# Optimization experiments

Hardware: AMD Instinct MI355X
Metric: run time of the kernel (lower is better)

The kernel has to match this reference:

```python
import jax, jax.numpy as jnp
import numpy as np

N = 50000
E = 600000
D = 128


def gcn_conv(x, row, col, w, W, b):
    """PyG GCNConv: add self-loops (weight 1), symmetric deg^-1/2 normalization,
    linear transform, edge-weighted scatter-add aggregation, then bias."""
    n = x.shape[0]
    loop = jnp.arange(n)
    r = jnp.concatenate([row, loop])            # source nodes, [E+N]
    c = jnp.concatenate([col, loop])            # target nodes, [E+N]
    ww = jnp.concatenate([w, jnp.ones((n,), x.dtype)])
    deg = jax.ops.segment_sum(ww, c, num_segments=n)          # weighted in-degree
    dinv = jnp.where(deg > 0, jax.lax.rsqrt(deg), jnp.zeros_like(deg))
    norm = dinv[r] * ww * dinv[c]               # [E+N]
    xl = x @ W                                  # [n, D_out]
    msg = norm[:, None] * xl[r]                 # gather + scale, [E+N, D_out]
    out = jax.ops.segment_sum(msg, c, num_segments=n)
    return out + b


def setup_inputs() -> dict:
    key = jax.random.key(0)
    ks = jax.random.split(key, 12)
    x = jax.random.normal(ks[0], (N, D), dtype=jnp.float32)
    edge_index = jax.random.randint(ks[1], (2, E), 0, N, dtype=jnp.int64)
    edge_weights = jax.random.uniform(ks[2], (E,), dtype=jnp.float32)
    s = 1.0 / np.sqrt(D)
    W1 = jax.random.uniform(ks[3], (D, D), jnp.float32, -s, s)
    b1 = jnp.zeros((D,), jnp.float32)
    W2 = jax.random.uniform(ks[4], (D, D), jnp.float32, -s, s)
    b2 = jnp.zeros((D,), jnp.float32)
    W3 = jax.random.uniform(ks[5], (D, D), jnp.float32, -s, s)
    b3 = jnp.zeros((D,), jnp.float32)
    prelu_w = jnp.array(0.25, jnp.float32)
    return {"x": x, "edge_index": edge_index, "edge_weights": edge_weights,
            "W1": W1, "b1": b1, "W2": W2, "b2": b2, "W3": W3, "b3": b3,
            "prelu_w": prelu_w}


def reference(x, edge_index, edge_weights, W1, b1, W2, b2, W3, b3, prelu_w):
    row, col = edge_index[0], edge_index[1]
    # layer 1: GCNConv -> (dropout: eval, identity) -> ELU
    h = gcn_conv(x, row, col, edge_weights, W1, b1)
    h = jax.nn.elu(h)
    # layer 2: GCNConv -> GELU (torch default = exact erf)
    h = gcn_conv(h, row, col, edge_weights, W2, b2)
    h = jax.nn.gelu(h, approximate=False)
    # layer 3: GCNConv -> PReLU (learnable scalar slope)
    h = gcn_conv(h, row, col, edge_weights, W3, b3)
    h = jnp.where(h >= 0, h, prelu_w * h)
    return h
```

## Files before the change

kernel.cpp:

```cpp
#include <hip/hip_runtime.h>
#include <hip/hip_fp16.h>
#include <math.h>

constexpr int D = 128;

struct __align__(16) H8 { __half2 h[4]; };
struct __align__(8)  H4 { __half2 a, b; };

typedef _Float16 half8 __attribute__((ext_vector_type(8)));
typedef float    floatx4 __attribute__((ext_vector_type(4)));


__device__ __forceinline__ int detect64(const int* __restrict__ ei) {
  int z = 0;
#pragma unroll
  for (int i = 0; i < 8; ++i) z |= ei[2 * i + 1];
  return (z == 0) ? 1 : 0;
}

__device__ __forceinline__ void load_edge(const int* __restrict__ ei, int e, int nE,
                                          int m64, int n, int& r, int& c) {
  if (m64) { r = ei[2 * (size_t)e]; c = ei[2 * ((size_t)nE + e)]; }
  else     { r = ei[(size_t)e];     c = ei[(size_t)nE + e]; }
  r = min(max(r, 0), n - 1);
  c = min(max(c, 0), n - 1);
}

__global__ void k_zero(int* __restrict__ cnt, int n) {
  int i = blockIdx.x * blockDim.x + threadIdx.x;
  if (i < n) cnt[i] = 0;
}

__global__ void k_pos(const int* __restrict__ ei, int* __restrict__ cnt,
                      int2* __restrict__ rc, int* __restrict__ pos, int nE, int n) {
  int e = blockIdx.x * blockDim.x + threadIdx.x;
  if (e >= nE) return;
  int m64 = detect64(ei);
  int r, c;
  load_edge(ei, e, nE, m64, n, r, c);
  rc[e] = make_int2(r, c);
  pos[e] = atomicAdd(&cnt[c], 1);
}

__global__ void k_scan1(const int* __restrict__ cnt, int* __restrict__ offs,
                        int* __restrict__ bsum, int n) {
  __shared__ int s[256];
  int t = threadIdx.x;
  int i = blockIdx.x * 256 + t;
  int v = (i < n) ? cnt[i] : 0;
  s[t] = v;
  __syncthreads();
  for (int off = 1; off < 256; off <<= 1) {
    int x = 0;
    if (t >= off) x = s[t - off];
    __syncthreads();
    if (t >= off) s[t] += x;
    __syncthreads();
  }
  if (i < n) offs[i] = s[t] - v;
  if (t == 255) bsum[blockIdx.x] = s[255];
}

__global__ void k_scan2(const int* __restrict__ bsum, int* __restrict__ boff, int nb) {
  __shared__ int s[256];
  int t = threadIdx.x;
  int v = (t < nb) ? bsum[t] : 0;
  s[t] = v;
  __syncthreads();
  for (int off = 1; off < 256; off <<= 1) {
    int x = 0;
    if (t >= off) x = s[t - off];
    __syncthreads();
    if (t >= off) s[t] += x;
    __syncthreads();
  }
  if (t < nb) boff[t] = s[t] - v;
}

__global__ void k_scan3(int* __restrict__ offs, const int* __restrict__ boff, int n, int nE) {
  int i = blockIdx.x * 256 + threadIdx.x;
  if (i < n) offs[i] += boff[blockIdx.x];
  if (i == 0) offs[n] = nE;
}

__global__ void k_fill(const int2* __restrict__ rc, const int* __restrict__ pos,
                       const float* __restrict__ w, const int* __restrict__ offs,
                       int2* __restrict__ ecf, int nE) {
  int e = blockIdx.x * blockDim.x + threadIdx.x;
  if (e >= nE) return;
  int2 p = rc[e];
  int idx = offs[p.y] + pos[e];
  ecf[idx] = make_int2(p.x, __float_as_int(w[e]));
}

__global__ void k_degdinv(const int2* __restrict__ ecf, const int* __restrict__ offs,
                          float* __restrict__ dinv, int n) {
  int i = blockIdx.x * blockDim.x + threadIdx.x;
  if (i >= n) return;
  float s = 1.0f;
  int e1 = offs[i + 1];
  for (int e = offs[i]; e < e1; ++e) s += __int_as_float(ecf[e].y);
  dinv[i] = rsqrtf(s);
}

__global__ void k_coef(const int2* __restrict__ ecf, const float* __restrict__ dinv,
                       unsigned int* __restrict__ ecf2, int nE) {
  int e = blockIdx.x * blockDim.x + threadIdx.x;
  if (e >= nE) return;
  int2 p = ecf[e];
  float c = dinv[p.x] * __int_as_float(p.y);
  ecf2[e] = ((unsigned int)p.x << 16) |
            (unsigned int)__half_as_ushort(__float2half_rn(c));
}

__global__ void k_wt(const float* __restrict__ W1, const float* __restrict__ W2,
                     const float* __restrict__ W3, __half* __restrict__ Wt) {
  __shared__ float s[128][129];
  const float* W = blockIdx.x == 0 ? W1 : (blockIdx.x == 1 ? W2 : W3);
  __half* o = Wt + (size_t)blockIdx.x * D * D;
  int tid = threadIdx.x;
#pragma unroll
  for (int i = 0; i < 16; ++i) {
    int flat = i * 1024 + tid * 4;
    int k = flat >> 7;
    int nn = flat & 127;
    float4 v = *(const float4*)(W + (size_t)k * D + nn);
    s[k][nn] = v.x; s[k][nn + 1] = v.y; s[k][nn + 2] = v.z; s[k][nn + 3] = v.w;
  }
  __syncthreads();
#pragma unroll
  for (int i = 0; i < 8; ++i) {
    int flat = i * 256 + tid;
    int nn = flat >> 4;
    int k0 = (flat & 15) * 8;
    H8 hv;
#pragma unroll
    for (int t = 0; t < 4; ++t)
      hv.h[t] = __floats2half2_rn(s[k0 + 2 * t][nn], s[k0 + 2 * t + 1][nn]);
    *(H8*)(o + (size_t)nn * D + k0) = hv;
  }
}

template <int ACT>
__device__ __forceinline__ float act_f(float x) {
  if (ACT == 1) return x > 0.f ? x : expm1f(x);
  if (ACT == 2) return 0.5f * x * (1.0f + erff(x * 0.70710678118654752440f));
  return x;
}

template <int ACT, typename AT>
__global__ __launch_bounds__(256) void k_gemm(const AT* __restrict__ A,
                                              const __half* __restrict__ Wt,
                                              __half* __restrict__ Y, int n) {
  const int wave = threadIdx.x >> 6;
  const int lane = threadIdx.x & 63;
  const int np = lane & 15;
  const int quad = lane >> 4;
  const int node = blockIdx.x * 64 + wave * 16 + np;
  const int nc = min(node, n - 1);

  half8 b[4];
#pragma unroll
  for (int s = 0; s < 4; ++s) {
    if constexpr (sizeof(AT) == 4) {
      const float* ap = (const float*)A + (size_t)nc * D + s * 32 + quad * 8;
      float4 v0 = *(const float4*)ap;
      float4 v1 = *(const float4*)(ap + 4);
      b[s][0] = (_Float16)act_f<ACT>(v0.x); b[s][1] = (_Float16)act_f<ACT>(v0.y);
      b[s][2] = (_Float16)act_f<ACT>(v0.z); b[s][3] = (_Float16)act_f<ACT>(v0.w);
      b[s][4] = (_Float16)act_f<ACT>(v1.x); b[s][5] = (_Float16)act_f<ACT>(v1.y);
      b[s][6] = (_Float16)act_f<ACT>(v1.z); b[s][7] = (_Float16)act_f<ACT>(v1.w);
    } else {
      half8 raw = *(const half8*)((const __half*)A + ((size_t)s * n + nc) * 32 + quad * 8);
#pragma unroll
      for (int t = 0; t < 8; ++t)
        b[s][t] = (_Float16)act_f<ACT>((float)raw[t]);
    }
  }

  floatx4 acc[8];
#pragma unroll
  for (int mt = 0; mt < 8; ++mt) acc[mt] = (floatx4){0.f, 0.f, 0.f, 0.f};

#pragma unroll
  for (int mt = 0; mt < 8; ++mt) {
#pragma unroll
    for (int s = 0; s < 4; ++s) {
      half8 a = *(const half8*)(Wt + (size_t)(mt * 16 + np) * D + s * 32 + quad * 8);
      acc[mt] = __builtin_amdgcn_mfma_f32_16x16x32_f16(a, b[s], acc[mt], 0, 0, 0);
    }
  }

  if (node < n) {
#pragma unroll
    for (int mt = 0; mt < 8; ++mt) {
      H4 hv;
      hv.a = __floats2half2_rn(acc[mt][0], acc[mt][1]);
      hv.b = __floats2half2_rn(acc[mt][2], acc[mt][3]);
      int f0 = mt * 16 + quad * 4;
      *(H4*)(Y + ((size_t)(f0 >> 5) * n + node) * 32 + (f0 & 31)) = hv;
    }
  }
}

__device__ __forceinline__ void fmacc8(float* acc, float c, const H8& y) {
  float2 f;
  f = __half22float2(y.h[0]); acc[0] += c * f.x; acc[1] += c * f.y;
  f = __half22float2(y.h[1]); acc[2] += c * f.x; acc[3] += c * f.y;
  f = __half22float2(y.h[2]); acc[4] += c * f.x; acc[5] += c * f.y;
  f = __half22float2(y.h[3]); acc[6] += c * f.x; acc[7] += c * f.y;
}

__device__ __forceinline__ float cdecode(unsigned int u) {
  return __half2float(__ushort_as_half((unsigned short)(u & 0xffffu)));
}

template <int PRELU, typename OutT>
__global__ __launch_bounds__(256) void k_agg(const __half* __restrict__ Y,
                                             const int* __restrict__ offs,
                                             const unsigned int* __restrict__ ecf2,
                                             const float* __restrict__ dinv,
                                             const float* __restrict__ bias,
                                             const float* __restrict__ pw,
                                             OutT* __restrict__ OUT, int n) {
  const int chunk = blockIdx.x & 3;
  const int t = threadIdx.x;
  const int node = (blockIdx.x >> 2) * 32 + (t >> 3);
  const int sub = (t >> 2) & 1;
  const int j = t & 3;
  if (node >= n) return;
  const __half* Yc = Y + (size_t)chunk * n * 32;
  float dc = dinv[node];
  float acc[8] = {0.f, 0.f, 0.f, 0.f, 0.f, 0.f, 0.f, 0.f};
  if (sub == 0) {
    H8 ys = *(const H8*)(Yc + (size_t)node * 32 + j * 8);
    fmacc8(acc, dc, ys);
  }
  int e0 = offs[node], e1 = offs[node + 1];
  int e = e0 + sub;
  for (; e + 6 < e1; e += 8) {
    unsigned int u0 = ecf2[e], u1 = ecf2[e + 2], u2 = ecf2[e + 4], u3 = ecf2[e + 6];
    H8 y0 = *(const H8*)(Yc + (size_t)(u0 >> 16) * 32 + j * 8);
    H8 y1 = *(const H8*)(Yc + (size_t)(u1 >> 16) * 32 + j * 8);
    H8 y2 = *(const H8*)(Yc + (size_t)(u2 >> 16) * 32 + j * 8);
    H8 y3 = *(const H8*)(Yc + (size_t)(u3 >> 16) * 32 + j * 8);
    fmacc8(acc, cdecode(u0), y0);
    fmacc8(acc, cdecode(u1), y1);
    fmacc8(acc, cdecode(u2), y2);
    fmacc8(acc, cdecode(u3), y3);
  }
  for (; e < e1; e += 2) {
    unsigned int u = ecf2[e];
    H8 y = *(const H8*)(Yc + (size_t)(u >> 16) * 32 + j * 8);
    fmacc8(acc, cdecode(u), y);
  }
#pragma unroll
  for (int i = 0; i < 8; ++i) acc[i] += __shfl_xor(acc[i], 4, 64);
  float4 b4 = *(const float4*)(bias + chunk * 32 + j * 8 + sub * 4);
  float o[4];
  o[0] = dc * acc[sub * 4 + 0] + b4.x;
  o[1] = dc * acc[sub * 4 + 1] + b4.y;
  o[2] = dc * acc[sub * 4 + 2] + b4.z;
  o[3] = dc * acc[sub * 4 + 3] + b4.w;
  if (PRELU) {
    float wv = *pw;
#pragma unroll
    for (int i = 0; i < 4; ++i) o[i] = o[i] >= 0.f ? o[i] : wv * o[i];
  }
  if constexpr (sizeof(OutT) == 4) {
    *(float4*)((float*)OUT + (size_t)node * D + chunk * 32 + j * 8 + sub * 4) =
        make_float4(o[0], o[1], o[2], o[3]);
  } else {
    H4 hv;
    hv.a = __floats2half2_rn(o[0], o[1]);
    hv.b = __floats2half2_rn(o[2], o[3]);
    *(H4*)((__half*)OUT + ((size_t)chunk * n + node) * 32 + j * 8 + sub * 4) = hv;
  }
}

extern "C" void kernel_launch(void* const* d_in, const int* in_sizes, int n_in,
                              void* d_out, int out_size, void* d_ws, size_t ws_size,
                              hipStream_t stream) {
  const float* x  = (const float*)d_in[0];
  const int*   ei = (const int*)d_in[1];
  const float* w  = (const float*)d_in[2];
  const float* W1 = (const float*)d_in[3];
  const float* b1 = (const float*)d_in[4];
  const float* W2 = (const float*)d_in[5];
  const float* b2 = (const float*)d_in[6];
  const float* W3 = (const float*)d_in[7];
  const float* b3 = (const float*)d_in[8];
  const float* pw = (const float*)d_in[9];
  const int N = in_sizes[0] / D;
  const int E = in_sizes[2];
  float* out = (float*)d_out;

  char* wsb = (char*)d_ws;
  size_t off = 0;
  auto alloc = [&](size_t bytes) {
    void* p = wsb + off;
    off = (off + bytes + 255) & ~(size_t)255;
    return p;
  };
  float*        dinv = (float*)alloc((size_t)N * 4);
  int*          cnt  = (int*)alloc((size_t)N * 4);
  int*          offs = (int*)alloc((size_t)(N + 1) * 4);
  int*          bsum = (int*)alloc(256 * 4);
  int*          boff = (int*)alloc(256 * 4);
  int2*         ecf  = (int2*)alloc((size_t)E * 8);
  unsigned int* ecf2 = (unsigned int*)alloc((size_t)E * 4);
  __half*       Wt   = (__half*)alloc((size_t)3 * D * D * 2);
  __half*       Y    = (__half*)alloc((size_t)N * D * 2);
  __half*       h    = (__half*)alloc((size_t)N * D * 2);
  int2*         rc   = (int2*)Y;
  int*          pos  = (int*)((char*)Y + (size_t)E * 8);

  const int nb = (N + 255) / 256;
  const int eb = (E + 255) / 256;

  hipLaunchKernelGGL(k_wt,      dim3(3),  dim3(256), 0, stream, W1, W2, W3, Wt);
  hipLaunchKernelGGL(k_zero,    dim3(nb), dim3(256), 0, stream, cnt, N);
  hipLaunchKernelGGL(k_pos,     dim3(eb), dim3(256), 0, stream, ei, cnt, rc, pos, E, N);
  hipLaunchKernelGGL(k_scan1,   dim3(nb), dim3(256), 0, stream, cnt, offs, bsum, N);
  hipLaunchKernelGGL(k_scan2,   dim3(1),  dim3(256), 0, stream, bsum, boff, nb);
  hipLaunchKernelGGL(k_scan3,   dim3(nb), dim3(256), 0, stream, offs, boff, N, E);
  hipLaunchKernelGGL(k_fill,    dim3(eb), dim3(256), 0, stream, rc, pos, w, offs, ecf, E);
  hipLaunchKernelGGL(k_degdinv, dim3(nb), dim3(256), 0, stream, ecf, offs, dinv, N);
  hipLaunchKernelGGL(k_coef,    dim3(eb), dim3(256), 0, stream, ecf, dinv, ecf2, E);

  const int gb = (N + 63) / 64;
  const int ab = 4 * ((N + 31) / 32);

  hipLaunchKernelGGL((k_gemm<0, float>),  dim3(gb), dim3(256), 0, stream, x, Wt,             Y, N);
  hipLaunchKernelGGL((k_agg<0, __half>),  dim3(ab), dim3(256), 0, stream, Y, offs, ecf2, dinv, b1, pw, h, N);
  hipLaunchKernelGGL((k_gemm<1, __half>), dim3(gb), dim3(256), 0, stream, h, Wt + D * D,     Y, N);
  hipLaunchKernelGGL((k_agg<0, __half>),  dim3(ab), dim3(256), 0, stream, Y, offs, ecf2, dinv, b2, pw, h, N);
  hipLaunchKernelGGL((k_gemm<2, __half>), dim3(gb), dim3(256), 0, stream, h, Wt + 2 * D * D, Y, N);
  hipLaunchKernelGGL((k_agg<1, float>),   dim3(ab), dim3(256), 0, stream, Y, offs, ecf2, dinv, b3, pw, out, N);
}
```

Measured before the change: 300.5 us.

## Fuse CSR preprocessing kernels, accumulate degree atomically, add nontemporal loads/stores

The preprocessing pipeline shrinks from nine launches to six. Weight transpose and counter zeroing share one kernel. The weighted degree is accumulated with float atomics during position counting, and dinv is computed inside the first scan pass. The CSR fill and coefficient packing are merged, which removes the intermediate ecf array and a pass over it. Separately, nontemporal loads and stores are added in the GEMM and aggregation kernels, and a 2-wide tail loop is added to aggregation. The trade-offs are extra atomic traffic on each edge and float-atomic ordering nondeterminism in the degree sum.

Result: slower. 350.1 us (+16.5%).

```diff
diff --git a/kernel.cpp b/kernel.cpp
--- a/kernel.cpp
+++ b/kernel.cpp
@@ -1,14 +1,45 @@
 #include <hip/hip_runtime.h>
 #include <hip/hip_fp16.h>
 #include <math.h>
+#include <string.h>
 
 constexpr int D = 128;
 
 struct __align__(16) H8 { __half2 h[4]; };
 struct __align__(8)  H4 { __half2 a, b; };
-
-typedef _Float16 half8 __attribute__((ext_vector_type(8)));
-typedef float    floatx4 __attribute__((ext_vector_type(4)));
+struct __align__(8)  CD { int cnt; float deg; };
+
+typedef _Float16 half8  __attribute__((ext_vector_type(8)));
+typedef float   floatx4 __attribute__((ext_vector_type(4)));
+typedef int     i32x4   __attribute__((ext_vector_type(4)));
+typedef int     i32x2   __attribute__((ext_vector_type(2)));
+
+template <typename T>
+__device__ __forceinline__ T ld_nt(const T* p) {
+  if constexpr (sizeof(T) == 16) {
+    i32x4 v = __builtin_nontemporal_load((const i32x4*)p);
+    T r; memcpy(&r, &v, 16); return r;
+  } else if constexpr (sizeof(T) == 8) {
+    i32x2 v = __builtin_nontemporal_load((const i32x2*)p);
+    T r; memcpy(&r, &v, 8); return r;
+  } else {
+    int v = __builtin_nontemporal_load((const int*)p);
+    T r; memcpy(&r, &v, 4); return r;
+  }
+}
+template <typename T>
+__device__ __forceinline__ void st_nt(T* p, T v) {
+  if constexpr (sizeof(T) == 16) {
+    i32x4 t; memcpy(&t, &v, 16);
+    __builtin_nontemporal_store(t, (i32x4*)p);
+  } else if constexpr (sizeof(T) == 8) {
+    i32x2 t; memcpy(&t, &v, 8);
+    __builtin_nontemporal_store(t, (i32x2*)p);
+  } else {
+    int t; memcpy(&t, &v, 4);
+    __builtin_nontemporal_store(t, (int*)p);
+  }
+}
 
 
 __device__ __forceinline__ int detect64(const int* __restrict__ ei) {
@@ -26,28 +57,68 @@
   c = min(max(c, 0), n - 1);
 }
 
-__global__ void k_zero(int* __restrict__ cnt, int n) {
-  int i = blockIdx.x * blockDim.x + threadIdx.x;
-  if (i < n) cnt[i] = 0;
-}
-
-__global__ void k_pos(const int* __restrict__ ei, int* __restrict__ cnt,
-                      int2* __restrict__ rc, int* __restrict__ pos, int nE, int n) {
-  int e = blockIdx.x * blockDim.x + threadIdx.x;
-  if (e >= nE) return;
+__global__ void k_init(const float* __restrict__ W1, const float* __restrict__ W2,
+                       const float* __restrict__ W3, __half* __restrict__ Wt,
+                       CD* __restrict__ cd, int n) {
+  __shared__ float s[128][129];
+  int tid = threadIdx.x;
+  if (blockIdx.x >= 3) {
+    int i = (blockIdx.x - 3) * 256 + tid;
+    if (i < n) *(long long*)&cd[i] = 0ll;
+    return;
+  }
+  const float* W = blockIdx.x == 0 ? W1 : (blockIdx.x == 1 ? W2 : W3);
+  __half* o = Wt + (size_t)blockIdx.x * D * D;
+#pragma unroll
+  for (int i = 0; i < 16; ++i) {
+    int flat = i * 1024 + tid * 4;
+    int k = flat >> 7;
+    int nn = flat & 127;
+    float4 v = *(const float4*)(W + (size_t)k * D + nn);
+    s[k][nn] = v.x; s[k][nn + 1] = v.y; s[k][nn + 2] = v.z; s[k][nn + 3] = v.w;
+  }
+  __syncthreads();
+#pragma unroll
+  for (int i = 0; i < 8; ++i) {
+    int flat = i * 256 + tid;
+    int nn = flat >> 4;
+    int k0 = (flat & 15) * 8;
+    H8 hv;
+#pragma unroll
+    for (int t = 0; t < 4; ++t)
+      hv.h[t] = __floats2half2_rn(s[k0 + 2 * t][nn], s[k0 + 2 * t + 1][nn]);
+    *(H8*)(o + (size_t)nn * D + k0) = hv;
+  }
+}
+
+__global__ void k_pos(const int* __restrict__ ei, const float* __restrict__ w,
+                      CD* __restrict__ cd, int2* __restrict__ rc,
+                      int* __restrict__ pos, int nE, int n) {
+  int base = (blockIdx.x * blockDim.x + threadIdx.x) * 2;
   int m64 = detect64(ei);
-  int r, c;
-  load_edge(ei, e, nE, m64, n, r, c);
-  rc[e] = make_int2(r, c);
-  pos[e] = atomicAdd(&cnt[c], 1);
-}
-
-__global__ void k_scan1(const int* __restrict__ cnt, int* __restrict__ offs,
-                        int* __restrict__ bsum, int n) {
+#pragma unroll
+  for (int u = 0; u < 2; ++u) {
+    int e = base + u;
+    if (e >= nE) break;
+    int r, c;
+    load_edge(ei, e, nE, m64, n, r, c);
+    rc[e] = make_int2(r, c);
+    pos[e] = atomicAdd(&cd[c].cnt, 1);
+    atomicAdd(&cd[c].deg, w[e]);
+  }
+}
+
+__global__ void k_scan1(const CD* __restrict__ cd, int* __restrict__ offs,
+                        int* __restrict__ bsum, float* __restrict__ dinv, int n) {
   __shared__ int s[256];
   int t = threadIdx.x;
   int i = blockIdx.x * 256 + t;
-  int v = (i < n) ? cnt[i] : 0;
+  int v = 0;
+  if (i < n) {
+    CD c = cd[i];
+    v = c.cnt;
+    dinv[i] = rsqrtf(1.0f + c.deg);
+  }
   s[t] = v;
   __syncthreads();
   for (int off = 1; off < 256; off <<= 1) {
@@ -83,61 +154,20 @@
   if (i == 0) offs[n] = nE;
 }
 
-__global__ void k_fill(const int2* __restrict__ rc, const int* __restrict__ pos,
-                       const float* __restrict__ w, const int* __restrict__ offs,
-                       int2* __restrict__ ecf, int nE) {
-  int e = blockIdx.x * blockDim.x + threadIdx.x;
-  if (e >= nE) return;
-  int2 p = rc[e];
-  int idx = offs[p.y] + pos[e];
-  ecf[idx] = make_int2(p.x, __float_as_int(w[e]));
-}
-
-__global__ void k_degdinv(const int2* __restrict__ ecf, const int* __restrict__ offs,
-                          float* __restrict__ dinv, int n) {
-  int i = blockIdx.x * blockDim.x + threadIdx.x;
-  if (i >= n) return;
-  float s = 1.0f;
-  int e1 = offs[i + 1];
-  for (int e = offs[i]; e < e1; ++e) s += __int_as_float(ecf[e].y);
-  dinv[i] = rsqrtf(s);
-}
-
-__global__ void k_coef(const int2* __restrict__ ecf, const float* __restrict__ dinv,
-                       unsigned int* __restrict__ ecf2, int nE) {
-  int e = blockIdx.x * blockDim.x + threadIdx.x;
-  if (e >= nE) return;
-  int2 p = ecf[e];
-  float c = dinv[p.x] * __int_as_float(p.y);
-  ecf2[e] = ((unsigned int)p.x << 16) |
-            (unsigned int)__half_as_ushort(__float2half_rn(c));
-}
-
-__global__ void k_wt(const float* __restrict__ W1, const float* __restrict__ W2,
-                     const float* __restrict__ W3, __half* __restrict__ Wt) {
-  __shared__ float s[128][129];
-  const float* W = blockIdx.x == 0 ? W1 : (blockIdx.x == 1 ? W2 : W3);
-  __half* o = Wt + (size_t)blockIdx.x * D * D;
-  int tid = threadIdx.x;
-#pragma unroll
-  for (int i = 0; i < 16; ++i) {
-    int flat = i * 1024 + tid * 4;
-    int k = flat >> 7;
-    int nn = flat & 127;
-    float4 v = *(const float4*)(W + (size_t)k * D + nn);
-    s[k][nn] = v.x; s[k][nn + 1] = v.y; s[k][nn + 2] = v.z; s[k][nn + 3] = v.w;
-  }
-  __syncthreads();
-#pragma unroll
-  for (int i = 0; i < 8; ++i) {
-    int flat = i * 256 + tid;
-    int nn = flat >> 4;
-    int k0 = (flat & 15) * 8;
-    H8 hv;
-#pragma unroll
-    for (int t = 0; t < 4; ++t)
-      hv.h[t] = __floats2half2_rn(s[k0 + 2 * t][nn], s[k0 + 2 * t + 1][nn]);
-    *(H8*)(o + (size_t)nn * D + k0) = hv;
+__global__ void k_fillcoef(const int2* __restrict__ rc, const int* __restrict__ pos,
+                           const float* __restrict__ w, const int* __restrict__ offs,
+                           const float* __restrict__ dinv,
+                           unsigned int* __restrict__ ecf2, int nE) {
+  int base = (blockIdx.x * blockDim.x + threadIdx.x) * 2;
+#pragma unroll
+  for (int u = 0; u < 2; ++u) {
+    int e = base + u;
+    if (e >= nE) break;
+    int2 p = rc[e];
+    int idx = offs[p.y] + pos[e];
+    float c = dinv[p.x] * w[e];
+    ecf2[idx] = ((unsigned int)p.x << 16) |
+                (unsigned int)__half_as_ushort(__float2half_rn(c));
   }
 }
 
@@ -164,14 +194,14 @@
   for (int s = 0; s < 4; ++s) {
     if constexpr (sizeof(AT) == 4) {
       const float* ap = (const float*)A + (size_t)nc * D + s * 32 + quad * 8;
-      float4 v0 = *(const float4*)ap;
-      float4 v1 = *(const float4*)(ap + 4);
+      float4 v0 = ld_nt((const float4*)ap);
+      float4 v1 = ld_nt((const float4*)(ap + 4));
       b[s][0] = (_Float16)act_f<ACT>(v0.x); b[s][1] = (_Float16)act_f<ACT>(v0.y);
       b[s][2] = (_Float16)act_f<ACT>(v0.z); b[s][3] = (_Float16)act_f<ACT>(v0.w);
       b[s][4] = (_Float16)act_f<ACT>(v1.x); b[s][5] = (_Float16)act_f<ACT>(v1.y);
       b[s][6] = (_Float16)act_f<ACT>(v1.z); b[s][7] = (_Float16)act_f<ACT>(v1.w);
     } else {
-      half8 raw = *(const half8*)((const __half*)A + ((size_t)s * n + nc) * 32 + quad * 8);
+      half8 raw = ld_nt((const half8*)((const __half*)A + ((size_t)s * n + nc) * 32 + quad * 8));
 #pragma unroll
       for (int t = 0; t < 8; ++t)
         b[s][t] = (_Float16)act_f<ACT>((float)raw[t]);
@@ -198,7 +228,7 @@
       hv.a = __floats2half2_rn(acc[mt][0], acc[mt][1]);
       hv.b = __floats2half2_rn(acc[mt][2], acc[mt][3]);
       int f0 = mt * 16 + quad * 4;
-      *(H4*)(Y + ((size_t)(f0 >> 5) * n + node) * 32 + (f0 & 31)) = hv;
+      st_nt((H4*)(Y + ((size_t)(f0 >> 5) * n + node) * 32 + (f0 & 31)), hv);
     }
   }
 }
@@ -239,7 +269,8 @@
   int e0 = offs[node], e1 = offs[node + 1];
   int e = e0 + sub;
   for (; e + 6 < e1; e += 8) {
-    unsigned int u0 = ecf2[e], u1 = ecf2[e + 2], u2 = ecf2[e + 4], u3 = ecf2[e + 6];
+    unsigned int u0 = ld_nt(&ecf2[e]),     u1 = ld_nt(&ecf2[e + 2]);
+    unsigned int u2 = ld_nt(&ecf2[e + 4]), u3 = ld_nt(&ecf2[e + 6]);
     H8 y0 = *(const H8*)(Yc + (size_t)(u0 >> 16) * 32 + j * 8);
     H8 y1 = *(const H8*)(Yc + (size_t)(u1 >> 16) * 32 + j * 8);
     H8 y2 = *(const H8*)(Yc + (size_t)(u2 >> 16) * 32 + j * 8);
@@ -249,8 +280,15 @@
     fmacc8(acc, cdecode(u2), y2);
     fmacc8(acc, cdecode(u3), y3);
   }
+  for (; e + 2 < e1; e += 4) {
+    unsigned int u0 = ld_nt(&ecf2[e]), u1 = ld_nt(&ecf2[e + 2]);
+    H8 y0 = *(const H8*)(Yc + (size_t)(u0 >> 16) * 32 + j * 8);
+    H8 y1 = *(const H8*)(Yc + (size_t)(u1 >> 16) * 32 + j * 8);
+    fmacc8(acc, cdecode(u0), y0);
+    fmacc8(acc, cdecode(u1), y1);
+  }
   for (; e < e1; e += 2) {
-    unsigned int u = ecf2[e];
+    unsigned int u = ld_nt(&ecf2[e]);
     H8 y = *(const H8*)(Yc + (size_t)(u >> 16) * 32 + j * 8);
     fmacc8(acc, cdecode(u), y);
   }
@@ -268,13 +306,13 @@
     for (int i = 0; i < 4; ++i) o[i] = o[i] >= 0.f ? o[i] : wv * o[i];
   }
   if constexpr (sizeof(OutT) == 4) {
-    *(float4*)((float*)OUT + (size_t)node * D + chunk * 32 + j * 8 + sub * 4) =
-        make_float4(o[0], o[1], o[2], o[3]);
+    st_nt((float4*)((float*)OUT + (size_t)node * D + chunk * 32 + j * 8 + sub * 4),
+          make_float4(o[0], o[1], o[2], o[3]));
   } else {
     H4 hv;
     hv.a = __floats2half2_rn(o[0], o[1]);
     hv.b = __floats2half2_rn(o[2], o[3]);
-    *(H4*)((__half*)OUT + ((size_t)chunk * n + node) * 32 + j * 8 + sub * 4) = hv;
+    st_nt((H4*)((__half*)OUT + ((size_t)chunk * n + node) * 32 + j * 8 + sub * 4), hv);
   }
 }
 
@@ -303,11 +341,10 @@
     return p;
   };
   float*        dinv = (float*)alloc((size_t)N * 4);
-  int*          cnt  = (int*)alloc((size_t)N * 4);
+  CD*           cd   = (CD*)alloc((size_t)N * 8);
   int*          offs = (int*)alloc((size_t)(N + 1) * 4);
   int*          bsum = (int*)alloc(256 * 4);
   int*          boff = (int*)alloc(256 * 4);
-  int2*         ecf  = (int2*)alloc((size_t)E * 8);
   unsigned int* ecf2 = (unsigned int*)alloc((size_t)E * 4);
   __half*       Wt   = (__half*)alloc((size_t)3 * D * D * 2);
   __half*       Y    = (__half*)alloc((size_t)N * D * 2);
@@ -315,18 +352,15 @@
   int2*         rc   = (int2*)Y;
   int*          pos  = (int*)((char*)Y + (size_t)E * 8);
 
-  const int nb = (N + 255) / 256;
-  const int eb = (E + 255) / 256;
-
-  hipLaunchKernelGGL(k_wt,      dim3(3),  dim3(256), 0, stream, W1, W2, W3, Wt);
-  hipLaunchKernelGGL(k_zero,    dim3(nb), dim3(256), 0, stream, cnt, N);
-  hipLaunchKernelGGL(k_pos,     dim3(eb), dim3(256), 0, stream, ei, cnt, rc, pos, E, N);
-  hipLaunchKernelGGL(k_scan1,   dim3(nb), dim3(256), 0, stream, cnt, offs, bsum, N);
-  hipLaunchKernelGGL(k_scan2,   dim3(1),  dim3(256), 0, stream, bsum, boff, nb);
-  hipLaunchKernelGGL(k_scan3,   dim3(nb), dim3(256), 0, stream, offs, boff, N, E);
-  hipLaunchKernelGGL(k_fill,    dim3(eb), dim3(256), 0, stream, rc, pos, w, offs, ecf, E);
-  hipLaunchKernelGGL(k_degdinv, dim3(nb), dim3(256), 0, stream, ecf, offs, dinv, N);
-  hipLaunchKernelGGL(k_coef,    dim3(eb), dim3(256), 0, stream, ecf, dinv, ecf2, E);
+  const int nb  = (N + 255) / 256;
+  const int eb2 = (E + 511) / 512;
+
+  hipLaunchKernelGGL(k_init,     dim3(3 + nb), dim3(256), 0, stream, W1, W2, W3, Wt, cd, N);
+  hipLaunchKernelGGL(k_pos,      dim3(eb2), dim3(256), 0, stream, ei, w, cd, rc, pos, E, N);
+  hipLaunchKernelGGL(k_scan1,    dim3(nb),  dim3(256), 0, stream, cd, offs, bsum, dinv, N);
+  hipLaunchKernelGGL(k_scan2,    dim3(1),   dim3(256), 0, stream, bsum, boff, nb);
+  hipLaunchKernelGGL(k_scan3,    dim3(nb),  dim3(256), 0, stream, offs, boff, N, E);
+  hipLaunchKernelGGL(k_fillcoef, dim3(eb2), dim3(256), 0, stream, rc, pos, w, offs, dinv, ecf2, E);
 
   const int gb = (N + 63) / 64;
   const int ab = 4 * ((N + 31) / 32);
```

## Merge init kernels, pack edge pairs, add nontemporal loads and extra unroll tier

Applied to the files above, without the earlier changes.

Merges the weight-transpose and count-zeroing kernels into one launch, which removes one kernel launch. Packs each (row, col) pair into one 16-bit+16-bit word to halve the temporary edge buffer traffic. Uses nontemporal loads for streamed edge coefficients and input features and a nontemporal store for the final output, to reduce cache pollution. Adds a 2-edge unrolled tail loop in the aggregation kernel. Packing limits node indices to 16 bits, which breaks for N=50000 unless values stay below 65536; they do, so the packing holds here.

After: 328.7 us. +9.4%, slower.

```diff
diff --git a/kernel.cpp b/kernel.cpp
--- a/kernel.cpp
+++ b/kernel.cpp
@@ -1,14 +1,31 @@
 #include <hip/hip_runtime.h>
 #include <hip/hip_fp16.h>
 #include <math.h>
+#include <string.h>
 
 constexpr int D = 128;
 
 struct __align__(16) H8 { __half2 h[4]; };
 struct __align__(8)  H4 { __half2 a, b; };
 
-typedef _Float16 half8 __attribute__((ext_vector_type(8)));
-typedef float    floatx4 __attribute__((ext_vector_type(4)));
+typedef _Float16 half8  __attribute__((ext_vector_type(8)));
+typedef float   floatx4 __attribute__((ext_vector_type(4)));
+typedef int     i32x4   __attribute__((ext_vector_type(4)));
+
+template <typename T>
+__device__ __forceinline__ T ld_nt(const T* p) {
+  if constexpr (sizeof(T) == 16) {
+    i32x4 v = __builtin_nontemporal_load((const i32x4*)p);
+    T r; memcpy(&r, &v, 16); return r;
+  } else {
+    int v = __builtin_nontemporal_load((const int*)p);
+    T r; memcpy(&r, &v, 4); return r;
+  }
+}
+__device__ __forceinline__ void st_nt16(void* p, float4 v) {
+  i32x4 t; memcpy(&t, &v, 16);
+  __builtin_nontemporal_store(t, (i32x4*)p);
+}
 
 
 __device__ __forceinline__ int detect64(const int* __restrict__ ei) {
@@ -26,19 +43,49 @@
   c = min(max(c, 0), n - 1);
 }
 
-__global__ void k_zero(int* __restrict__ cnt, int n) {
-  int i = blockIdx.x * blockDim.x + threadIdx.x;
-  if (i < n) cnt[i] = 0;
+__global__ void k_init(const float* __restrict__ W1, const float* __restrict__ W2,
+                       const float* __restrict__ W3, __half* __restrict__ Wt,
+                       int* __restrict__ cnt, int n) {
+  __shared__ float s[128][129];
+  int tid = threadIdx.x;
+  if (blockIdx.x >= 3) {
+    int i = (blockIdx.x - 3) * 256 + tid;
+    if (i < n) cnt[i] = 0;
+    return;
+  }
+  const float* W = blockIdx.x == 0 ? W1 : (blockIdx.x == 1 ? W2 : W3);
+  __half* o = Wt + (size_t)blockIdx.x * D * D;
+#pragma unroll
+  for (int i = 0; i < 16; ++i) {
+    int flat = i * 1024 + tid * 4;
+    int k = flat >> 7;
+    int nn = flat & 127;
+    float4 v = *(const float4*)(W + (size_t)k * D + nn);
+    s[k][nn] = v.x; s[k][nn + 1] = v.y; s[k][nn + 2] = v.z; s[k][nn + 3] = v.w;
+  }
+  __syncthreads();
+#pragma unroll
+  for (int i = 0; i < 8; ++i) {
+    int flat = i * 256 + tid;
+    int nn = flat >> 4;
+    int k0 = (flat & 15) * 8;
+    H8 hv;
+#pragma unroll
+    for (int t = 0; t < 4; ++t)
+      hv.h[t] = __floats2half2_rn(s[k0 + 2 * t][nn], s[k0 + 2 * t + 1][nn]);
+    *(H8*)(o + (size_t)nn * D + k0) = hv;
+  }
 }
 
 __global__ void k_pos(const int* __restrict__ ei, int* __restrict__ cnt,
-                      int2* __restrict__ rc, int* __restrict__ pos, int nE, int n) {
+                      unsigned int* __restrict__ rcp, int* __restrict__ pos,
+                      int nE, int n) {
   int e = blockIdx.x * blockDim.x + threadIdx.x;
   if (e >= nE) return;
   int m64 = detect64(ei);
   int r, c;
   load_edge(ei, e, nE, m64, n, r, c);
-  rc[e] = make_int2(r, c);
+  rcp[e] = ((unsigned int)r << 16) | (unsigned int)c;
   pos[e] = atomicAdd(&cnt[c], 1);
 }
 
@@ -83,14 +130,14 @@
   if (i == 0) offs[n] = nE;
 }
 
-__global__ void k_fill(const int2* __restrict__ rc, const int* __restrict__ pos,
+__global__ void k_fill(const unsigned int* __restrict__ rcp, const int* __restrict__ pos,
                        const float* __restrict__ w, const int* __restrict__ offs,
                        int2* __restrict__ ecf, int nE) {
   int e = blockIdx.x * blockDim.x + threadIdx.x;
   if (e >= nE) return;
-  int2 p = rc[e];
-  int idx = offs[p.y] + pos[e];
-  ecf[idx] = make_int2(p.x, __float_as_int(w[e]));
+  unsigned int p = rcp[e];
+  int idx = offs[p & 0xffffu] + pos[e];
+  ecf[idx] = make_int2((int)(p >> 16), __float_as_int(w[e]));
 }
 
 __global__ void k_degdinv(const int2* __restrict__ ecf, const int* __restrict__ offs,
@@ -111,34 +158,6 @@
   float c = dinv[p.x] * __int_as_float(p.y);
   ecf2[e] = ((unsigned int)p.x << 16) |
             (unsigned int)__half_as_ushort(__float2half_rn(c));
-}
-
-__global__ void k_wt(const float* __restrict__ W1, const float* __restrict__ W2,
-                     const float* __restrict__ W3, __half* __restrict__ Wt) {
-  __shared__ float s[128][129];
-  const float* W = blockIdx.x == 0 ? W1 : (blockIdx.x == 1 ? W2 : W3);
-  __half* o = Wt + (size_t)blockIdx.x * D * D;
-  int tid = threadIdx.x;
-#pragma unroll
-  for (int i = 0; i < 16; ++i) {
-    int flat = i * 1024 + tid * 4;
-    int k = flat >> 7;
-    int nn = flat & 127;
-    float4 v = *(const float4*)(W + (size_t)k * D + nn);
-    s[k][nn] = v.x; s[k][nn + 1] = v.y; s[k][nn + 2] = v.z; s[k][nn + 3] = v.w;
-  }
-  __syncthreads();
-#pragma unroll
-  for (int i = 0; i < 8; ++i) {
-    int flat = i * 256 + tid;
-    int nn = flat >> 4;
-    int k0 = (flat & 15) * 8;
-    H8 hv;
-#pragma unroll
-    for (int t = 0; t < 4; ++t)
-      hv.h[t] = __floats2half2_rn(s[k0 + 2 * t][nn], s[k0 + 2 * t + 1][nn]);
-    *(H8*)(o + (size_t)nn * D + k0) = hv;
-  }
 }
 
 template <int ACT>
@@ -164,8 +183,8 @@
   for (int s = 0; s < 4; ++s) {
     if constexpr (sizeof(AT) == 4) {
       const float* ap = (const float*)A + (size_t)nc * D + s * 32 + quad * 8;
-      float4 v0 = *(const float4*)ap;
-      float4 v1 = *(const float4*)(ap + 4);
+      float4 v0 = ld_nt((const float4*)ap);
+      float4 v1 = ld_nt((const float4*)(ap + 4));
       b[s][0] = (_Float16)act_f<ACT>(v0.x); b[s][1] = (_Float16)act_f<ACT>(v0.y);
       b[s][2] = (_Float16)act_f<ACT>(v0.z); b[s][3] = (_Float16)act_f<ACT>(v0.w);
       b[s][4] = (_Float16)act_f<ACT>(v1.x); b[s][5] = (_Float16)act_f<ACT>(v1.y);
@@ -239,7 +258,8 @@
   int e0 = offs[node], e1 = offs[node + 1];
   int e = e0 + sub;
   for (; e + 6 < e1; e += 8) {
-    unsigned int u0 = ecf2[e], u1 = ecf2[e + 2], u2 = ecf2[e + 4], u3 = ecf2[e + 6];
+    unsigned int u0 = ld_nt(&ecf2[e]),     u1 = ld_nt(&ecf2[e + 2]);
+    unsigned int u2 = ld_nt(&ecf2[e + 4]), u3 = ld_nt(&ecf2[e + 6]);
     H8 y0 = *(const H8*)(Yc + (size_t)(u0 >> 16) * 32 + j * 8);
     H8 y1 = *(const H8*)(Yc + (size_t)(u1 >> 16) * 32 + j * 8);
     H8 y2 = *(const H8*)(Yc + (size_t)(u2 >> 16) * 32 + j * 8);
@@ -249,8 +269,15 @@
     fmacc8(acc, cdecode(u2), y2);
     fmacc8(acc, cdecode(u3), y3);
   }
+  for (; e + 2 < e1; e += 4) {
+    unsigned int u0 = ld_nt(&ecf2[e]), u1 = ld_nt(&ecf2[e + 2]);
+    H8 y0 = *(const H8*)(Yc + (size_t)(u0 >> 16) * 32 + j * 8);
+    H8 y1 = *(const H8*)(Yc + (size_t)(u1 >> 16) * 32 + j * 8);
+    fmacc8(acc, cdecode(u0), y0);
+    fmacc8(acc, cdecode(u1), y1);
+  }
   for (; e < e1; e += 2) {
-    unsigned int u = ecf2[e];
+    unsigned int u = ld_nt(&ecf2[e]);
     H8 y = *(const H8*)(Yc + (size_t)(u >> 16) * 32 + j * 8);
     fmacc8(acc, cdecode(u), y);
   }
@@ -268,8 +295,8 @@
     for (int i = 0; i < 4; ++i) o[i] = o[i] >= 0.f ? o[i] : wv * o[i];
   }
   if constexpr (sizeof(OutT) == 4) {
-    *(float4*)((float*)OUT + (size_t)node * D + chunk * 32 + j * 8 + sub * 4) =
-        make_float4(o[0], o[1], o[2], o[3]);
+    st_nt16((float*)OUT + (size_t)node * D + chunk * 32 + j * 8 + sub * 4,
+            make_float4(o[0], o[1], o[2], o[3]));
   } else {
     H4 hv;
     hv.a = __floats2half2_rn(o[0], o[1]);
@@ -312,19 +339,18 @@
   __half*       Wt   = (__half*)alloc((size_t)3 * D * D * 2);
   __half*       Y    = (__half*)alloc((size_t)N * D * 2);
   __half*       h    = (__half*)alloc((size_t)N * D * 2);
-  int2*         rc   = (int2*)Y;
-  int*          pos  = (int*)((char*)Y + (size_t)E * 8);
+  unsigned int* rcp  = (unsigned int*)Y;
+  int*          pos  = (int*)((char*)Y + (size_t)E * 4);
 
   const int nb = (N + 255) / 256;
   const int eb = (E + 255) / 256;
 
-  hipLaunchKernelGGL(k_wt,      dim3(3),  dim3(256), 0, stream, W1, W2, W3, Wt);
-  hipLaunchKernelGGL(k_zero,    dim3(nb), dim3(256), 0, stream, cnt, N);
-  hipLaunchKernelGGL(k_pos,     dim3(eb), dim3(256), 0, stream, ei, cnt, rc, pos, E, N);
+  hipLaunchKernelGGL(k_init,    dim3(3 + nb), dim3(256), 0, stream, W1, W2, W3, Wt, cnt, N);
+  hipLaunchKernelGGL(k_pos,     dim3(eb), dim3(256), 0, stream, ei, cnt, rcp, pos, E, N);
   hipLaunchKernelGGL(k_scan1,   dim3(nb), dim3(256), 0, stream, cnt, offs, bsum, N);
   hipLaunchKernelGGL(k_scan2,   dim3(1),  dim3(256), 0, stream, bsum, boff, nb);
   hipLaunchKernelGGL(k_scan3,   dim3(nb), dim3(256), 0, stream, offs, boff, N, E);
-  hipLaunchKernelGGL(k_fill,    dim3(eb), dim3(256), 0, stream, rc, pos, w, offs, ecf, E);
+  hipLaunchKernelGGL(k_fill,    dim3(eb), dim3(256), 0, stream, rcp, pos, w, offs, ecf, E);
   hipLaunchKernelGGL(k_degdinv, dim3(nb), dim3(256), 0, stream, ecf, offs, dinv, N);
   hipLaunchKernelGGL(k_coef,    dim3(eb), dim3(256), 0, stream, ecf, dinv, ecf2, E);
 
```
